# Kernel optimization log

Measured on AMD Instinct MI355X. Metric: run time of the kernel, lower is better.

Reference implementation:

```python
import jax, jax.numpy as jnp
import numpy as np

B, S, D, HW = 256, 32, 512, 196


def setup_inputs() -> dict:
    key = jax.random.key(0)
    ks = jax.random.split(key, 34)
    n = lambda k, sh, s=1.0: jax.random.normal(k, sh, dtype=jnp.float32) * s
    w = 0.03  # xavier-ish scale for D=512 layers
    return {
        "words": n(ks[0], (B, S, D)),
        "question": n(ks[1], (B, 2 * D)),
        "know": n(ks[2], (B, D, HW)),
        "control0": n(ks[3], (B, D)),
        "memory0": n(ks[4], (B, D)),
        # ControlUnit
        "Wsc": n(ks[5], (2 * D, D), w), "bsc": jnp.zeros((D,), jnp.float32),
        "Wp": n(ks[6], (D, D), w), "bp": jnp.zeros((D,), jnp.float32),
        "Wcq": n(ks[7], (2 * D, D), w), "bcq": jnp.zeros((D,), jnp.float32),
        "wac": n(ks[8], (D, 1), w), "bac": jnp.zeros((1,), jnp.float32),
        # ReadUnit
        "Wm": n(ks[9], (D, D), w), "bm": jnp.zeros((D,), jnp.float32),
        "Wk": n(ks[10], (D, D), w), "bk": jnp.zeros((D,), jnp.float32),
        "Wc1": n(ks[11], (3 * D, D), w), "bc1": jnp.zeros((D,), jnp.float32),
        "Wc2": n(ks[12], (D, D), w), "bc2": jnp.zeros((D,), jnp.float32),
        "war": n(ks[13], (D, 1), w), "bar": jnp.zeros((1,), jnp.float32),
        # WriteUnit (self-attention variant)
        "Wwc": n(ks[14], (D, D), w), "bwc": jnp.zeros((D,), jnp.float32),
        "waw": n(ks[15], (D, 1), w), "baw": jnp.zeros((1,), jnp.float32),
        "Wwcat": n(ks[16], (3 * D, D), w), "bwcat": jnp.zeros((D,), jnp.float32),
    }


def reference(words, question, know, control0, memory0,
              Wsc, bsc, Wp, bp, Wcq, bcq, wac, bac,
              Wm, bm, Wk, bk, Wc1, bc1, Wc2, bc2, war, bar,
              Wwc, bwc, waw, baw, Wwcat, bwcat):
    # ---- ControlUnit (step 0) ----
    q = jnp.tanh(question @ Wsc + bsc)                    # [B,D]
    pa = q @ Wp + bp                                      # position_aware[0]
    cq = jnp.concatenate([control0, pa], axis=1) @ Wcq + bcq  # [B,D]
    logit_c = (cq[:, None, :] * words) @ wac + bac        # [B,S,1]
    attn_c = jax.nn.softmax(logit_c, axis=1)
    control = jnp.sum(attn_c * words, axis=1)             # [B,D]

    # ---- ReadUnit ----
    pm = memory0 @ Wm + bm                                # [B,D]
    pk = jnp.einsum('bdn,de->ben', know, Wk) + bk[None, :, None]  # [B,D,HW]
    pm_b = jnp.broadcast_to(pm[:, :, None], pk.shape)
    feat = jnp.concatenate([pm_b * pk, pk, pm_b], axis=1)  # [B,3D,HW]
    h = jax.nn.relu(jnp.einsum('bfn,fd->bnd', feat, Wc1) + bc1)  # [B,HW,D]
    h = h @ Wc2 + bc2                                     # [B,HW,D]
    logit_r = (h * control[:, None, :]) @ war + bar       # [B,HW,1]
    a_r = jax.nn.softmax(logit_r[..., 0], axis=1)          # [B,HW]
    read = jnp.einsum('bdn,bn->bd', know, a_r)            # [B,D]

    # ---- WriteUnit (self-attention over previous controls; T=1 at step 0) ----
    sc = control @ Wwc + bwc                              # [B,D]
    ctrl_prev = control0[:, :, None]                      # [B,D,T]
    logit_w = jnp.einsum('bdt,d->bt', sc[:, :, None] * ctrl_prev, waw[:, 0]) + baw  # [B,T]
    a_w = jax.nn.softmax(logit_w, axis=1)
    attn_mem = jnp.einsum('bdt,bt->bd', memory0[:, :, None], a_w)  # [B,D]
    concat = jnp.concatenate([read, memory0, attn_mem], axis=1)    # [B,3D]
    next_mem = concat @ Wwcat + bwcat                     # [B,D]

    return control, next_mem
```

## Files before the change

### kernel.cpp

```cpp
#include <hip/hip_runtime.h>
#include <hip/hip_bf16.h>
#include <math.h>

typedef __hip_bfloat16 bf16;
typedef __attribute__((ext_vector_type(8))) short s8v;
typedef __attribute__((ext_vector_type(4))) short s4v;
typedef __attribute__((ext_vector_type(4))) float f4v;

#define BB 256
#define SS 32
#define DD 512
#define HWN 196
#define APW 72

__device__ __forceinline__ float b2f(bf16 x){ return __bfloat162float(x); }
__device__ __forceinline__ bf16 f2b(float x){ return __float2bfloat16(x); }
__device__ __forceinline__ float us2f(unsigned short u){
    union { unsigned int i; float f; } t; t.i = ((unsigned int)u) << 16; return t.f;
}
__device__ __forceinline__ float ldin(int dt, const void* p, size_t i){
    return dt ? b2f(((const bf16*)p)[i]) : ((const float*)p)[i];
}

__global__ void detect_k(const void* q, int* flag){
    __shared__ int cnt;
    if (threadIdx.x == 0) cnt = 0;
    __syncthreads();
    const unsigned short* u = (const unsigned short*)q;
    unsigned short v = u[threadIdx.x * 4];
    int e = (v >> 7) & 0xFF;
    atomicAdd(&cnt, (e >= 100 && e <= 140) ? 1 : 0);
    __syncthreads();
    if (threadIdx.x == 0) *flag = (cnt > 128) ? 1 : 0;
}

struct PJob { const void* s; const void* s_b; const void* s2; const void* s2_b;
              bf16* d; int R, C, ldd, kofs, mode, boff; };
struct PrepP { PJob j[11]; const void* war; const void* bk; float* warf; float* bkf; };

__global__ __launch_bounds__(256) void prep_k(PrepP P, const int* __restrict__ flag){
    const int dt = *flag;
    __shared__ float T[32][33];
    int bx = blockIdx.x;
    int ji = 0;
    #pragma unroll
    for (int i = 0; i < 11; ++i) if (bx >= P.j[i].boff) ji = i;
    PJob jb = P.j[ji];
    const void* src  = dt ? jb.s_b  : jb.s;
    const void* src2 = dt ? jb.s2_b : jb.s2;
    int t = bx - jb.boff;
    int tx = threadIdx.x & 31, ty = threadIdx.x >> 5;
    if (jb.mode == 3){
        for (int i = threadIdx.x; i < DD; i += 256){
            P.warf[i] = ldin(dt, P.war, i);
            P.bkf[i]  = ldin(dt, P.bk, i);
        }
        return;
    }
    int nrt = jb.R >> 5;
    int r0 = (t % nrt) << 5, c0 = (t / nrt) << 5;
    if (jb.mode == 2){
        for (int rr = ty; rr < 32; rr += 8)
            jb.d[(size_t)(r0 + rr) * jb.ldd + jb.kofs + c0 + tx] =
                f2b(ldin(dt, src, (size_t)(r0 + rr) * jb.C + c0 + tx));
        return;
    }
    for (int rr = ty; rr < 32; rr += 8){
        float v = ldin(dt, src, (size_t)(r0 + rr) * jb.C + c0 + tx);
        if (jb.mode == 1) v += ldin(dt, src2, (size_t)(r0 + rr) * jb.C + c0 + tx);
        T[rr][tx] = v;
    }
    __syncthreads();
    for (int rr = ty; rr < 32; rr += 8)
        jb.d[(size_t)(c0 + rr) * jb.ldd + jb.kofs + r0 + tx] = f2b(T[tx][rr]);
}

__global__ __launch_bounds__(256) void g1_mfma(const void* __restrict__ know,
                                               const bf16* __restrict__ BT,
                                               const float* __restrict__ bkf,
                                               bf16* __restrict__ C,
                                               int b0, int swz,
                                               const int* __restrict__ flag){
    const int dt = *flag;
    __shared__ __align__(16) bf16 As[128 * APW];
    __shared__ __align__(16) bf16 Bs[128 * APW];
    const int tid = threadIdx.x, lane = tid & 63, wave = tid >> 6;
    const int q = lane >> 4, mr = lane & 15;
    int idb = blockIdx.x, rt, ct;
    if (swz){ int g = idb >> 5, w = idb & 31; rt = g * 8 + (w & 7); ct = w >> 3; }
    else    { rt = idb >> 2; ct = idb & 3; }
    const int r0 = rt * 128, c0 = ct * 128;
    const int quad = tid >> 3;
    const int kg   = tid & 7;
    const int m    = r0 + quad * 4;
    const int bl   = m / HWN;
    const int n    = m - bl * HWN;
    const size_t abase = ((size_t)(b0 + bl) * DD) * HWN + n;
    f4v acc[2][8];
    #pragma unroll
    for (int t = 0; t < 2; ++t)
        #pragma unroll
        for (int j = 0; j < 8; ++j){ f4v z = {0.f,0.f,0.f,0.f}; acc[t][j] = z; }
    for (int k0 = 0; k0 < DD; k0 += 64){
        #pragma unroll
        for (int h = 0; h < 2; ++h){
            int kb = k0 + h * 32 + kg * 4;
            union { bf16 hh[4]; s4v v; } pk_[4];
            if (dt == 0){
                const float* kp = (const float*)know + abase + (size_t)kb * HWN;
                float4 ra  = *(const float4*)kp;
                float4 rb  = *(const float4*)(kp + HWN);
                float4 rc  = *(const float4*)(kp + 2 * HWN);
                float4 rd4 = *(const float4*)(kp + 3 * HWN);
                #pragma unroll
                for (int j = 0; j < 4; ++j){
                    pk_[j].hh[0] = f2b((&ra.x)[j]);
                    pk_[j].hh[1] = f2b((&rb.x)[j]);
                    pk_[j].hh[2] = f2b((&rc.x)[j]);
                    pk_[j].hh[3] = f2b((&rd4.x)[j]);
                }
            } else {
                const unsigned short* kp = (const unsigned short*)know + abase + (size_t)kb * HWN;
                ushort4 ua = *(const ushort4*)kp;
                ushort4 ub = *(const ushort4*)(kp + HWN);
                ushort4 uc = *(const ushort4*)(kp + 2 * HWN);
                ushort4 ud = *(const ushort4*)(kp + 3 * HWN);
                #pragma unroll
                for (int j = 0; j < 4; ++j){
                    ((unsigned short*)&pk_[j].v)[0] = (&ua.x)[j];
                    ((unsigned short*)&pk_[j].v)[1] = (&ub.x)[j];
                    ((unsigned short*)&pk_[j].v)[2] = (&uc.x)[j];
                    ((unsigned short*)&pk_[j].v)[3] = (&ud.x)[j];
                }
            }
            #pragma unroll
            for (int j = 0; j < 4; ++j)
                *(s4v*)&As[(quad * 4 + j) * APW + h * 32 + kg * 4] = pk_[j].v;
        }
        {
            int col = tid >> 1, kb = (tid & 1) * 32;
            const bf16* wp = BT + (size_t)(c0 + col) * DD + k0 + kb;
            bf16* dst = &Bs[col * APW + kb];
            #pragma unroll
            for (int t4 = 0; t4 < 32; t4 += 8)
                *(float4*)(dst + t4) = *(const float4*)(wp + t4);
        }
        __syncthreads();
        #pragma unroll
        for (int h = 0; h < 2; ++h){
            s8v a0 = *(const s8v*)&As[(wave * 32 + mr) * APW + h * 32 + q * 8];
            s8v a1 = *(const s8v*)&As[(wave * 32 + 16 + mr) * APW + h * 32 + q * 8];
            #pragma unroll
            for (int j = 0; j < 8; ++j){
                s8v b = *(const s8v*)&Bs[(j * 16 + mr) * APW + h * 32 + q * 8];
                acc[0][j] = __builtin_amdgcn_mfma_f32_16x16x32_bf16(a0, b, acc[0][j], 0, 0, 0);
                acc[1][j] = __builtin_amdgcn_mfma_f32_16x16x32_bf16(a1, b, acc[1][j], 0, 0, 0);
            }
        }
        __syncthreads();
    }
    #pragma unroll
    for (int t = 0; t < 2; ++t)
        #pragma unroll
        for (int j = 0; j < 8; ++j){
            float bb = bkf[c0 + j * 16 + mr];
            #pragma unroll
            for (int i = 0; i < 4; ++i){
                int row = r0 + wave * 32 + t * 16 + q * 4 + i;
                int col = c0 + j * 16 + mr;
                C[(size_t)row * DD + col] = f2b(acc[t][j][i] + bb);
            }
        }
}

__global__ __launch_bounds__(256) void g2_mfma(const bf16* __restrict__ Apk,
                                               const bf16* __restrict__ BT,
                                               const float* __restrict__ pmf,
                                               const float* __restrict__ t3b,
                                               const float* __restrict__ uf,
                                               float* __restrict__ lpart,
                                               int b0, int swz){
    __shared__ __align__(16) bf16 As[128 * APW];
    __shared__ __align__(16) bf16 Bs[128 * APW];
    const int tid = threadIdx.x, lane = tid & 63, wave = tid >> 6;
    const int q = lane >> 4, mr = lane & 15;
    int idb = blockIdx.x, u, ct;
    if (swz){ int g = idb >> 5, w = idb & 31; u = g * 8 + (w & 7); ct = w >> 3; }
    else    { u = idb >> 2; ct = idb & 3; }
    const int bl = u >> 1, rt = u & 1;
    const int b = b0 + bl;
    const int c0 = ct * 128, rbase = rt * 128;
    const float* pmb = pmf + (size_t)b * DD;
    f4v acc[2][8];
    #pragma unroll
    for (int t = 0; t < 2; ++t)
        #pragma unroll
        for (int j = 0; j < 8; ++j){ f4v z = {0.f,0.f,0.f,0.f}; acc[t][j] = z; }
    for (int k0 = 0; k0 < DD; k0 += 64){
        {
            int row = tid >> 1, kb = (tid & 1) * 32;
            int rl = rbase + row;
            bf16* dst = &As[row * APW + kb];
            if (rl < HWN){
                const bf16* ap = Apk + ((size_t)bl * HWN + rl) * DD + k0 + kb;
                #pragma unroll
                for (int t4 = 0; t4 < 32; t4 += 8)
                    *(float4*)(dst + t4) = *(const float4*)(ap + t4);
            } else {
                float4 z = {0.f,0.f,0.f,0.f};
                #pragma unroll
                for (int t4 = 0; t4 < 32; t4 += 8)
                    *(float4*)(dst + t4) = z;
            }
        }
        {
            int col = tid >> 1, kb = (tid & 1) * 32;
            const bf16* wrow = BT + (size_t)(c0 + col) * (2 * DD) + k0 + kb;
            bf16* dst = &Bs[col * APW + kb];
            #pragma unroll
            for (int t4 = 0; t4 < 32; t4 += 8){
                union { bf16 h[8]; float4 f; } w1, w2, be;
                w1.f = *(const float4*)(wrow + t4);
                w2.f = *(const float4*)(wrow + DD + t4);
                float4 pA = *(const float4*)(pmb + k0 + kb + t4);
                float4 pB = *(const float4*)(pmb + k0 + kb + t4 + 4);
                #pragma unroll
                for (int j = 0; j < 4; ++j){
                    be.h[j]     = f2b((&pA.x)[j] * b2f(w1.h[j])     + b2f(w2.h[j]));
                    be.h[4 + j] = f2b((&pB.x)[j] * b2f(w1.h[4 + j]) + b2f(w2.h[4 + j]));
                }
                *(float4*)(dst + t4) = be.f;
            }
        }
        __syncthreads();
        #pragma unroll
        for (int h = 0; h < 2; ++h){
            s8v a0 = *(const s8v*)&As[(wave * 32 + mr) * APW + h * 32 + q * 8];
            s8v a1 = *(const s8v*)&As[(wave * 32 + 16 + mr) * APW + h * 32 + q * 8];
            #pragma unroll
            for (int j = 0; j < 8; ++j){
                s8v b2 = *(const s8v*)&Bs[(j * 16 + mr) * APW + h * 32 + q * 8];
                acc[0][j] = __builtin_amdgcn_mfma_f32_16x16x32_bf16(a0, b2, acc[0][j], 0, 0, 0);
                acc[1][j] = __builtin_amdgcn_mfma_f32_16x16x32_bf16(a1, b2, acc[1][j], 0, 0, 0);
            }
        }
        __syncthreads();
    }
    float part[2][4] = {};
    #pragma unroll
    for (int t = 0; t < 2; ++t)
        #pragma unroll
        for (int j = 0; j < 8; ++j)
            #pragma unroll
            for (int i = 0; i < 4; ++i){
                int rl = rbase + wave * 32 + t * 16 + q * 4 + i;
                if (rl < HWN){
                    int col = c0 + j * 16 + mr;
                    float hv = acc[t][j][i] + t3b[(size_t)b * DD + col];
                    part[t][i] += fmaxf(hv, 0.f) * uf[(size_t)b * DD + col];
                }
            }
    #pragma unroll
    for (int t = 0; t < 2; ++t)
        #pragma unroll
        for (int i = 0; i < 4; ++i){
            float v = part[t][i];
            v += __shfl_xor(v, 1, 16);
            v += __shfl_xor(v, 2, 16);
            v += __shfl_xor(v, 4, 16);
            v += __shfl_xor(v, 8, 16);
            int rl = rbase + wave * 32 + t * 16 + q * 4 + i;
            if (mr == 0 && rl < HWN)
                lpart[(size_t)ct * (BB * HWN) + (size_t)b * HWN + rl] = v;
        }
}

struct SSeg { const void* A; int a_ws, lda, K, koff; };
struct SP {
    SSeg s[2]; int nseg;
    const bf16* BT; int ldb;
    const float* amul;
    const void* bias;
    float* C; int M, N, act;
    void* out2; int o2off;
};
struct SPP { SP j[2]; };

__global__ __launch_bounds__(256) void sgemm_k(SPP P, const int* __restrict__ flag){
    const int dt = *flag;
    const SP p = P.j[blockIdx.z];
    const int tid = threadIdx.x, lane = tid & 63, w = tid >> 6;
    const int q = lane >> 4, mr = lane & 15;
    const int n0 = blockIdx.x * 16, m0 = blockIdx.y * 64 + w * 16;
    f4v acc = {0.f,0.f,0.f,0.f};
    for (int sg = 0; sg < p.nseg; ++sg){
        const SSeg s = p.s[sg];
        const float* amul = (sg == 0) ? p.amul : nullptr;
        #pragma unroll 4
        for (int k0 = 0; k0 < s.K; k0 += 32){
            const int kk = k0 + q * 8;
            union { bf16 h[8]; s8v v; } a;
            if (s.a_ws || dt == 0){
                const float* Af = (const float*)s.A + (size_t)(m0 + mr) * s.lda + kk;
                float4 f0 = *(const float4*)Af;
                float4 f1 = *(const float4*)(Af + 4);
                float f[8] = {f0.x, f0.y, f0.z, f0.w, f1.x, f1.y, f1.z, f1.w};
                if (amul){
                    #pragma unroll
                    for (int j = 0; j < 8; ++j) f[j] *= amul[kk + j];
                }
                #pragma unroll
                for (int j = 0; j < 8; ++j) a.h[j] = f2b(f[j]);
            } else {
                a.v = *(const s8v*)((const bf16*)s.A + (size_t)(m0 + mr) * s.lda + kk);
                if (amul){
                    #pragma unroll
                    for (int j = 0; j < 8; ++j) a.h[j] = f2b(b2f(a.h[j]) * amul[kk + j]);
                }
            }
            s8v b = *(const s8v*)(p.BT + (size_t)(n0 + mr) * p.ldb + s.koff + kk);
            acc = __builtin_amdgcn_mfma_f32_16x16x32_bf16(a.v, b, acc, 0, 0, 0);
        }
    }
    #pragma unroll
    for (int i = 0; i < 4; ++i){
        int row = m0 + q * 4 + i, col = n0 + mr;
        float v = acc[i] + (p.bias ? ldin(dt, p.bias, col) : 0.f);
        if (p.act == 1) v = tanhf(v);
        p.C[(size_t)row * p.N + col] = v;
        if (p.out2){
            size_t oi = (size_t)p.o2off + (size_t)row * p.N + col;
            if (dt) ((bf16*)p.out2)[oi] = f2b(v);
            else    ((float*)p.out2)[oi] = v;
        }
    }
}

__global__ __launch_bounds__(256) void attn_control_k(const float* __restrict__ cq,
                                                      const void* __restrict__ wac,
                                                      const void* __restrict__ bac,
                                                      const void* __restrict__ words,
                                                      float* __restrict__ control,
                                                      const void* __restrict__ bc2,
                                                      const float* __restrict__ warf,
                                                      const void* __restrict__ bar,
                                                      float* __restrict__ bias_r,
                                                      void* __restrict__ out,
                                                      const int* __restrict__ flag){
    extern __shared__ float wl[];
    const int dt = *flag;
    const int b = blockIdx.x, tid = threadIdx.x;
    __shared__ float cw[DD];
    __shared__ float lg[SS];
    __shared__ float es[SS];
    __shared__ float red[256];
    for (int i = tid; i < SS * DD; i += 256)
        wl[i] = ldin(dt, words, (size_t)b * SS * DD + i);
    for (int d = tid; d < DD; d += 256) cw[d] = cq[(size_t)b*DD + d] * ldin(dt, wac, d);
    __syncthreads();
    int s = tid >> 3, l8 = tid & 7;
    float p = 0.f;
    for (int d = l8; d < DD; d += 8) p += cw[d] * wl[s * DD + d];
    for (int off = 4; off; off >>= 1) p += __shfl_down(p, off, 8);
    if (l8 == 0) lg[s] = p + ldin(dt, bac, 0);
    __syncthreads();
    if (tid < SS){
        float x = lg[tid];
        float mx = x;
        #pragma unroll
        for (int off = 16; off; off >>= 1) mx = fmaxf(mx, __shfl_xor(mx, off, 32));
        float e = expf(x - mx);
        float sm = e;
        #pragma unroll
        for (int off = 16; off; off >>= 1) sm += __shfl_xor(sm, off, 32);
        es[tid] = e / sm;
    }
    __syncthreads();
    float vb = 0.f;
    for (int d = tid; d < DD; d += 256){
        float c = 0.f;
        #pragma unroll 8
        for (int s2 = 0; s2 < SS; ++s2) c += es[s2] * wl[s2 * DD + d];
        control[(size_t)b*DD + d] = c;
        if (dt) ((bf16*)out)[(size_t)b*DD + d] = f2b(c);
        else    ((float*)out)[(size_t)b*DD + d] = c;
        vb += ldin(dt, bc2, d) * c * warf[d];
    }
    red[tid] = vb; __syncthreads();
    for (int off = 128; off; off >>= 1){ if (tid < off) red[tid] += red[tid + off]; __syncthreads(); }
    if (tid == 0) bias_r[b] = red[0] + ldin(dt, bar, 0);
}

__global__ __launch_bounds__(256) void softmax_read_k(const float* __restrict__ lpart,
                                                      const float* __restrict__ bias_r,
                                                      const void* __restrict__ know,
                                                      float* __restrict__ readout,
                                                      const int* __restrict__ flag){
    const int dt = *flag;
    const int b = blockIdx.x, tid = threadIdx.x;
    __shared__ float a[HWN];
    __shared__ float red[256];
    float x = -INFINITY;
    if (tid < HWN){
        float sacc = bias_r[b];
        #pragma unroll
        for (int c = 0; c < 4; ++c)
            sacc += lpart[(size_t)c * (BB * HWN) + (size_t)b * HWN + tid];
        x = sacc;
    }
    red[tid] = x; __syncthreads();
    for (int off = 128; off; off >>= 1){ if (tid < off) red[tid] = fmaxf(red[tid], red[tid + off]); __syncthreads(); }
    float mx = red[0]; __syncthreads();
    float e = (tid < HWN) ? expf(x - mx) : 0.f;
    red[tid] = e; __syncthreads();
    for (int off = 128; off; off >>= 1){ if (tid < off) red[tid] += red[tid + off]; __syncthreads(); }
    float inv = 1.f / red[0];
    if (tid < HWN) a[tid] = e * inv;
    __syncthreads();
    for (int d = tid; d < DD; d += 256){
        size_t base = ((size_t)b*DD + d) * HWN;
        float sum = 0.f;
        if (dt){
            const ushort4* k4 = (const ushort4*)((const unsigned short*)know + base);
            #pragma unroll 7
            for (int c = 0; c < HWN/4; ++c){
                ushort4 u4 = k4[c];
                sum += a[4*c+0]*us2f(u4.x) + a[4*c+1]*us2f(u4.y)
                     + a[4*c+2]*us2f(u4.z) + a[4*c+3]*us2f(u4.w);
            }
        } else {
            const float4* k4 = (const float4*)((const float*)know + base);
            #pragma unroll 7
            for (int c = 0; c < HWN/4; ++c){
                float4 f4 = k4[c];
                sum += a[4*c+0]*f4.x + a[4*c+1]*f4.y + a[4*c+2]*f4.z + a[4*c+3]*f4.w;
            }
        }
        readout[(size_t)b*DD + d] = sum;
    }
}

extern "C" void kernel_launch(void* const* d_in, const int* in_sizes, int n_in,
                              void* d_out, int out_size, void* d_ws, size_t ws_size,
                              hipStream_t stream){
    const void* words    = d_in[0];
    const void* question = d_in[1];
    const void* know     = d_in[2];
    const void* control0 = d_in[3];
    const void* memory0  = d_in[4];
    const void* Wsc = d_in[5];   const void* bsc = d_in[6];
    const void* Wp  = d_in[7];   const void* bp  = d_in[8];
    const void* Wcq = d_in[9];   const void* bcq = d_in[10];
    const void* wac = d_in[11];  const void* bac = d_in[12];
    const void* Wm  = d_in[13];  const void* bm  = d_in[14];
    const void* Wk  = d_in[15];  const void* bk  = d_in[16];
    const void* Wc1 = d_in[17];  const void* bc1 = d_in[18];
    const void* Wc2 = d_in[19];  const void* bc2 = d_in[20];
    const void* war = d_in[21];  const void* bar = d_in[22];
    const void* Wwcat = d_in[27]; const void* bwcat = d_in[28];

    int* flag = (int*)d_ws;
    float* F = ((float*)d_ws) + 16;
    const int NBD = BB * DD;
    float* q_   = F;
    float* pa   = F + 1*NBD;
    float* cq   = F + 2*NBD;
    float* ctrl = F + 3*NBD;
    float* pm   = F + 4*NBD;
    float* t3b  = F + 5*NBD;
    float* u_   = F + 6*NBD;
    float* rd   = F + 7*NBD;
    float* nm   = F + 8*NBD;
    float* bias_r = F + 9*NBD;
    float* warf   = bias_r + BB;
    float* bkf    = warf + DD;
    float* lpart  = bkf + DD;
    size_t off_f = 16 + 9*(size_t)NBD + BB + 2*DD + 8*(size_t)BB*HWN;
    size_t byte_off = (off_f * 4 + 255) & ~(size_t)255;
    bf16* WB = (bf16*)((char*)d_ws + byte_off);
    bf16* WscT   = WB;
    bf16* WcqT   = WscT  + (size_t)DD*2*DD;
    bf16* Wc1T2  = WcqT  + (size_t)DD*2*DD;
    bf16* WwcatF = Wc1T2 + (size_t)DD*2*DD;
    bf16* WpT    = WwcatF+ (size_t)DD*2*DD;
    bf16* WmT    = WpT   + (size_t)DD*DD;
    bf16* Wc1t3T = WmT   + (size_t)DD*DD;
    bf16* WkT    = Wc1t3T+ (size_t)DD*DD;
    bf16* Wc2cv  = WkT   + (size_t)DD*DD;
    size_t big_off = (byte_off + ((size_t)DD*2*DD*4 + (size_t)DD*DD*5) * sizeof(bf16) + 255) & ~(size_t)255;

    size_t per_batch = (size_t)HWN * DD * sizeof(bf16);
    size_t avail = (ws_size > big_off) ? (ws_size - big_off) : 0;
    int CB = (int)(avail / per_batch);
    CB &= ~31;
    if (CB > BB) CB = BB;
    if (CB < 32) CB = 32;
    bf16* pkT = (bf16*)((char*)d_ws + big_off);

    dim3 blk(256);

    {
        const int q_f32 = BB * 2 * DD * 4;
        const int q_b16 = BB * 2 * DD * 2;
        if (in_sizes[1] == q_f32)      (void)hipMemsetAsync(flag, 0, 4, stream);
        else if (in_sizes[1] == q_b16) (void)hipMemsetAsync(flag, 1, 4, stream);
        else detect_k<<<dim3(1), blk, 0, stream>>>(question, flag);
    }

    {
        PrepP P; int bo = 0;
        auto J = [&](const void* s, const void* sb, const void* s2, const void* s2b,
                     bf16* d, int R, int C, int ldd, int kofs, int mode, int idx){
            int nb = (mode == 3) ? 1 : ((R >> 5) * (C >> 5));
            P.j[idx] = PJob{ s, sb, s2, s2b, d, R, C, ldd, kofs, mode, bo };
            bo += nb;
        };
        const void* Wc1t3_f = (const void*)((const float*)Wc1 + (size_t)2*DD*DD);
        const void* Wc1t3_b = (const void*)((const bf16*) Wc1 + (size_t)2*DD*DD);
        const void* Ww1_f = (const void*)((const float*)Wwcat + (size_t)DD*DD);
        const void* Ww1_b = (const void*)((const bf16*) Wwcat + (size_t)DD*DD);
        const void* Ww2_f = (const void*)((const float*)Wwcat + (size_t)2*DD*DD);
        const void* Ww2_b = (const void*)((const bf16*) Wwcat + (size_t)2*DD*DD);
        J(Wsc,   Wsc,   nullptr, nullptr, WscT,   2*DD, DD, 2*DD, 0,   0, 0);
        J(Wp,    Wp,    nullptr, nullptr, WpT,    DD,   DD, DD,   0,   0, 1);
        J(Wcq,   Wcq,   nullptr, nullptr, WcqT,   2*DD, DD, 2*DD, 0,   0, 2);
        J(Wm,    Wm,    nullptr, nullptr, WmT,    DD,   DD, DD,   0,   0, 3);
        J(Wc1,   Wc1,   nullptr, nullptr, Wc1T2,  2*DD, DD, 2*DD, 0,   0, 4);
        J(Wc1t3_f, Wc1t3_b, nullptr, nullptr, Wc1t3T, DD, DD, DD, 0,   0, 5);
        J(Wk,    Wk,    nullptr, nullptr, WkT,    DD,   DD, DD,   0,   0, 6);
        J(Wwcat, Wwcat, nullptr, nullptr, WwcatF, DD,   DD, 2*DD, 0,   0, 7);
        J(Ww1_f, Ww1_b, Ww2_f,   Ww2_b,   WwcatF, DD,   DD, 2*DD, 512, 1, 8);
        J(Wc2,   Wc2,   nullptr, nullptr, Wc2cv,  DD,   DD, DD,   0,   2, 9);
        J(nullptr,nullptr,nullptr,nullptr,nullptr,0,    0,  0,    0,   3, 10);
        P.war = war; P.bk = bk; P.warf = warf; P.bkf = bkf;
        prep_k<<<dim3(bo), blk, 0, stream>>>(P, flag);
    }

    SPP P2;
    auto mkjob = [&](SP& p){ p = SP{}; };

    mkjob(P2.j[0]);
    P2.j[0].nseg = 1;
    P2.j[0].s[0] = SSeg{ question, 0, 2*DD, 2*DD, 0 };
    P2.j[0].BT = WscT; P2.j[0].ldb = 2*DD;
    P2.j[0].bias = bsc; P2.j[0].C = q_; P2.j[0].M = BB; P2.j[0].N = DD; P2.j[0].act = 1;
    mkjob(P2.j[1]);
    P2.j[1].nseg = 1;
    P2.j[1].s[0] = SSeg{ memory0, 0, DD, DD, 0 };
    P2.j[1].BT = WmT; P2.j[1].ldb = DD;
    P2.j[1].bias = bm; P2.j[1].C = pm; P2.j[1].M = BB; P2.j[1].N = DD; P2.j[1].act = 0;
    sgemm_k<<<dim3(DD/16, BB/64, 2), blk, 0, stream>>>(P2, flag);

    mkjob(P2.j[0]);
    P2.j[0].nseg = 1;
    P2.j[0].s[0] = SSeg{ q_, 1, DD, DD, 0 };
    P2.j[0].BT = WpT; P2.j[0].ldb = DD;
    P2.j[0].bias = bp; P2.j[0].C = pa; P2.j[0].M = BB; P2.j[0].N = DD; P2.j[0].act = 0;
    mkjob(P2.j[1]);
    P2.j[1].nseg = 1;
    P2.j[1].s[0] = SSeg{ pm, 1, DD, DD, 0 };
    P2.j[1].BT = Wc1t3T; P2.j[1].ldb = DD;
    P2.j[1].bias = bc1; P2.j[1].C = t3b; P2.j[1].M = BB; P2.j[1].N = DD; P2.j[1].act = 0;
    sgemm_k<<<dim3(DD/16, BB/64, 2), blk, 0, stream>>>(P2, flag);

    mkjob(P2.j[0]);
    P2.j[0].nseg = 2;
    P2.j[0].s[0] = SSeg{ control0, 0, DD, DD, 0 };
    P2.j[0].s[1] = SSeg{ pa,       1, DD, DD, 512 };
    P2.j[0].BT = WcqT; P2.j[0].ldb = 2*DD;
    P2.j[0].bias = bcq; P2.j[0].C = cq; P2.j[0].M = BB; P2.j[0].N = DD; P2.j[0].act = 0;
    sgemm_k<<<dim3(DD/16, BB/64, 1), blk, 0, stream>>>(P2, flag);

    {
        static bool attr_set = false;
        const int attn_lds = SS * DD * 4;
        if (!attr_set){
            (void)hipFuncSetAttribute(reinterpret_cast<const void*>(attn_control_k),
                                      hipFuncAttributeMaxDynamicSharedMemorySize, attn_lds);
            attr_set = true;
        }
        attn_control_k<<<dim3(BB), blk, attn_lds, stream>>>(cq, wac, bac, words, ctrl,
                                                            bc2, warf, bar, bias_r, d_out, flag);
    }

    mkjob(P2.j[0]);
    P2.j[0].nseg = 1;
    P2.j[0].s[0] = SSeg{ ctrl, 1, DD, DD, 0 };
    P2.j[0].BT = Wc2cv; P2.j[0].ldb = DD; P2.j[0].amul = warf;
    P2.j[0].C = u_; P2.j[0].M = BB; P2.j[0].N = DD; P2.j[0].act = 0;
    sgemm_k<<<dim3(DD/16, BB/64, 1), blk, 0, stream>>>(P2, flag);

    for (int b0 = 0; b0 < BB; b0 += CB){
        int cb = (b0 + CB <= BB) ? CB : (BB - b0);
        int M = cb * HWN;
        int nR = M / 128;
        int swz1 = (nR % 8 == 0) ? 1 : 0;
        g1_mfma<<<dim3(4 * nR), blk, 0, stream>>>(know, WkT, bkf, pkT, b0, swz1, flag);
        int nU = cb * 2;
        int swz2 = (nU % 8 == 0) ? 1 : 0;
        g2_mfma<<<dim3(4 * nU), blk, 0, stream>>>(pkT, Wc1T2, pm, t3b, u_, lpart, b0, swz2);
    }

    softmax_read_k<<<dim3(BB), blk, 0, stream>>>(lpart, bias_r, know, rd, flag);

    mkjob(P2.j[0]);
    P2.j[0].nseg = 2;
    P2.j[0].s[0] = SSeg{ rd,      1, DD, DD, 0 };
    P2.j[0].s[1] = SSeg{ memory0, 0, DD, DD, 512 };
    P2.j[0].BT = WwcatF; P2.j[0].ldb = 2*DD;
    P2.j[0].bias = bwcat; P2.j[0].C = nm; P2.j[0].M = BB; P2.j[0].N = DD; P2.j[0].act = 0;
    P2.j[0].out2 = d_out; P2.j[0].o2off = NBD;
    sgemm_k<<<dim3(DD/16, BB/64, 1), blk, 0, stream>>>(P2, flag);
}
```

Baseline: 559.1 us.

## XOR-swizzle MFMA LDS tiles and split softmax-read across channel blocks

Replaces the padded LDS layout (row stride 72) in both MFMA GEMM kernels with an unpadded 64-wide layout using an XOR swizzle on 16-byte slots, so tile reads and writes avoid bank conflicts while using less shared memory. Separately, softmax_read_k now launches 8 blocks per batch along y. Each block stages a 64-channel slice of know into LDS and reduces it with 4 threads per channel plus shuffles, instead of one thread streaming a whole 196-element row. The cost is that every y-block recomputes the softmax, and the 50KB LDS staging buffer limits occupancy.

```diff
diff --git a/kernel.cpp b/kernel.cpp
--- a/kernel.cpp
+++ b/kernel.cpp
@@ -11,7 +11,6 @@
 #define SS 32
 #define DD 512
 #define HWN 196
-#define APW 72
 
 __device__ __forceinline__ float b2f(bf16 x){ return __bfloat162float(x); }
 __device__ __forceinline__ bf16 f2b(float x){ return __float2bfloat16(x); }
@@ -20,6 +19,9 @@
 }
 __device__ __forceinline__ float ldin(int dt, const void* p, size_t i){
     return dt ? b2f(((const bf16*)p)[i]) : ((const float*)p)[i];
+}
+__device__ __forceinline__ int swz(int row, int slot){
+    return row * 64 + ((slot ^ (row & 7)) << 3);
 }
 
 __global__ void detect_k(const void* q, int* flag){
@@ -79,16 +81,16 @@
                                                const bf16* __restrict__ BT,
                                                const float* __restrict__ bkf,
                                                bf16* __restrict__ C,
-                                               int b0, int swz,
+                                               int b0, int swzb,
                                                const int* __restrict__ flag){
     const int dt = *flag;
-    __shared__ __align__(16) bf16 As[128 * APW];
-    __shared__ __align__(16) bf16 Bs[128 * APW];
+    __shared__ __align__(16) bf16 As[128 * 64];
+    __shared__ __align__(16) bf16 Bs[128 * 64];
     const int tid = threadIdx.x, lane = tid & 63, wave = tid >> 6;
     const int q = lane >> 4, mr = lane & 15;
     int idb = blockIdx.x, rt, ct;
-    if (swz){ int g = idb >> 5, w = idb & 31; rt = g * 8 + (w & 7); ct = w >> 3; }
-    else    { rt = idb >> 2; ct = idb & 3; }
+    if (swzb){ int g = idb >> 5, w = idb & 31; rt = g * 8 + (w & 7); ct = w >> 3; }
+    else     { rt = idb >> 2; ct = idb & 3; }
     const int r0 = rt * 128, c0 = ct * 128;
     const int quad = tid >> 3;
     const int kg   = tid & 7;
@@ -133,26 +135,28 @@
                     ((unsigned short*)&pk_[j].v)[3] = (&ud.x)[j];
                 }
             }
+            const int slot = h * 4 + (kg >> 1);
+            const int sub  = (kg & 1) * 4;
             #pragma unroll
             for (int j = 0; j < 4; ++j)
-                *(s4v*)&As[(quad * 4 + j) * APW + h * 32 + kg * 4] = pk_[j].v;
+                *(s4v*)&As[swz(quad * 4 + j, slot) + sub] = pk_[j].v;
         }
         {
-            int col = tid >> 1, kb = (tid & 1) * 32;
-            const bf16* wp = BT + (size_t)(c0 + col) * DD + k0 + kb;
-            bf16* dst = &Bs[col * APW + kb];
+            const int col = tid >> 1, sb = (tid & 1) * 4;
+            const bf16* wp = BT + (size_t)(c0 + col) * DD + k0 + (tid & 1) * 32;
             #pragma unroll
-            for (int t4 = 0; t4 < 32; t4 += 8)
-                *(float4*)(dst + t4) = *(const float4*)(wp + t4);
+            for (int t4 = 0; t4 < 4; ++t4)
+                *(float4*)&Bs[swz(col, sb + t4)] = *(const float4*)(wp + t4 * 8);
         }
         __syncthreads();
         #pragma unroll
         for (int h = 0; h < 2; ++h){
-            s8v a0 = *(const s8v*)&As[(wave * 32 + mr) * APW + h * 32 + q * 8];
-            s8v a1 = *(const s8v*)&As[(wave * 32 + 16 + mr) * APW + h * 32 + q * 8];
+            const int slot = h * 4 + q;
+            s8v a0 = *(const s8v*)&As[swz(wave * 32 + mr, slot)];
+            s8v a1 = *(const s8v*)&As[swz(wave * 32 + 16 + mr, slot)];
             #pragma unroll
             for (int j = 0; j < 8; ++j){
-                s8v b = *(const s8v*)&Bs[(j * 16 + mr) * APW + h * 32 + q * 8];
+                s8v b = *(const s8v*)&Bs[swz(j * 16 + mr, slot)];
                 acc[0][j] = __builtin_amdgcn_mfma_f32_16x16x32_bf16(a0, b, acc[0][j], 0, 0, 0);
                 acc[1][j] = __builtin_amdgcn_mfma_f32_16x16x32_bf16(a1, b, acc[1][j], 0, 0, 0);
             }
@@ -179,14 +183,14 @@
                                                const float* __restrict__ t3b,
                                                const float* __restrict__ uf,
                                                float* __restrict__ lpart,
-                                               int b0, int swz){
-    __shared__ __align__(16) bf16 As[128 * APW];
-    __shared__ __align__(16) bf16 Bs[128 * APW];
+                                               int b0, int swzb){
+    __shared__ __align__(16) bf16 As[128 * 64];
+    __shared__ __align__(16) bf16 Bs[128 * 64];
     const int tid = threadIdx.x, lane = tid & 63, wave = tid >> 6;
     const int q = lane >> 4, mr = lane & 15;
     int idb = blockIdx.x, u, ct;
-    if (swz){ int g = idb >> 5, w = idb & 31; u = g * 8 + (w & 7); ct = w >> 3; }
-    else    { u = idb >> 2; ct = idb & 3; }
+    if (swzb){ int g = idb >> 5, w = idb & 31; u = g * 8 + (w & 7); ct = w >> 3; }
+    else     { u = idb >> 2; ct = idb & 3; }
     const int bl = u >> 1, rt = u & 1;
     const int b = b0 + bl;
     const int c0 = ct * 128, rbase = rt * 128;
@@ -198,48 +202,48 @@
         for (int j = 0; j < 8; ++j){ f4v z = {0.f,0.f,0.f,0.f}; acc[t][j] = z; }
     for (int k0 = 0; k0 < DD; k0 += 64){
         {
-            int row = tid >> 1, kb = (tid & 1) * 32;
-            int rl = rbase + row;
-            bf16* dst = &As[row * APW + kb];
+            const int row = tid >> 1, sb = (tid & 1) * 4;
+            const int rl = rbase + row;
             if (rl < HWN){
-                const bf16* ap = Apk + ((size_t)bl * HWN + rl) * DD + k0 + kb;
+                const bf16* ap = Apk + ((size_t)bl * HWN + rl) * DD + k0 + (tid & 1) * 32;
                 #pragma unroll
-                for (int t4 = 0; t4 < 32; t4 += 8)
-                    *(float4*)(dst + t4) = *(const float4*)(ap + t4);
+                for (int t4 = 0; t4 < 4; ++t4)
+                    *(float4*)&As[swz(row, sb + t4)] = *(const float4*)(ap + t4 * 8);
             } else {
                 float4 z = {0.f,0.f,0.f,0.f};
                 #pragma unroll
-                for (int t4 = 0; t4 < 32; t4 += 8)
-                    *(float4*)(dst + t4) = z;
+                for (int t4 = 0; t4 < 4; ++t4)
+                    *(float4*)&As[swz(row, sb + t4)] = z;
             }
         }
         {
-            int col = tid >> 1, kb = (tid & 1) * 32;
-            const bf16* wrow = BT + (size_t)(c0 + col) * (2 * DD) + k0 + kb;
-            bf16* dst = &Bs[col * APW + kb];
+            const int col = tid >> 1, sb = (tid & 1) * 4;
+            const int kb = k0 + (tid & 1) * 32;
+            const bf16* wrow = BT + (size_t)(c0 + col) * (2 * DD) + kb;
             #pragma unroll
-            for (int t4 = 0; t4 < 32; t4 += 8){
+            for (int t4 = 0; t4 < 4; ++t4){
                 union { bf16 h[8]; float4 f; } w1, w2, be;
-                w1.f = *(const float4*)(wrow + t4);
-                w2.f = *(const float4*)(wrow + DD + t4);
-                float4 pA = *(const float4*)(pmb + k0 + kb + t4);
-                float4 pB = *(const float4*)(pmb + k0 + kb + t4 + 4);
+                w1.f = *(const float4*)(wrow + t4 * 8);
+                w2.f = *(const float4*)(wrow + DD + t4 * 8);
+                float4 pA = *(const float4*)(pmb + kb + t4 * 8);
+                float4 pB = *(const float4*)(pmb + kb + t4 * 8 + 4);
                 #pragma unroll
                 for (int j = 0; j < 4; ++j){
                     be.h[j]     = f2b((&pA.x)[j] * b2f(w1.h[j])     + b2f(w2.h[j]));
                     be.h[4 + j] = f2b((&pB.x)[j] * b2f(w1.h[4 + j]) + b2f(w2.h[4 + j]));
                 }
-                *(float4*)(dst + t4) = be.f;
+                *(float4*)&Bs[swz(col, sb + t4)] = be.f;
             }
         }
         __syncthreads();
         #pragma unroll
         for (int h = 0; h < 2; ++h){
-            s8v a0 = *(const s8v*)&As[(wave * 32 + mr) * APW + h * 32 + q * 8];
-            s8v a1 = *(const s8v*)&As[(wave * 32 + 16 + mr) * APW + h * 32 + q * 8];
+            const int slot = h * 4 + q;
+            s8v a0 = *(const s8v*)&As[swz(wave * 32 + mr, slot)];
+            s8v a1 = *(const s8v*)&As[swz(wave * 32 + 16 + mr, slot)];
             #pragma unroll
             for (int j = 0; j < 8; ++j){
-                s8v b2 = *(const s8v*)&Bs[(j * 16 + mr) * APW + h * 32 + q * 8];
+                s8v b2 = *(const s8v*)&Bs[swz(j * 16 + mr, slot)];
                 acc[0][j] = __builtin_amdgcn_mfma_f32_16x16x32_bf16(a0, b2, acc[0][j], 0, 0, 0);
                 acc[1][j] = __builtin_amdgcn_mfma_f32_16x16x32_bf16(a1, b2, acc[1][j], 0, 0, 0);
             }
@@ -397,9 +401,10 @@
                                                       float* __restrict__ readout,
                                                       const int* __restrict__ flag){
     const int dt = *flag;
-    const int b = blockIdx.x, tid = threadIdx.x;
+    const int b = blockIdx.x, ch = blockIdx.y, tid = threadIdx.x;
     __shared__ float a[HWN];
     __shared__ float red[256];
+    __shared__ float kl[64 * HWN];
     float x = -INFINITY;
     if (tid < HWN){
         float sacc = bias_r[b];
@@ -416,28 +421,31 @@
     for (int off = 128; off; off >>= 1){ if (tid < off) red[tid] += red[tid + off]; __syncthreads(); }
     float inv = 1.f / red[0];
     if (tid < HWN) a[tid] = e * inv;
+    const int d0 = ch * 64;
+    const size_t gbase = ((size_t)b * DD + d0) * HWN;
+    if (dt){
+        const ushort4* src = (const ushort4*)((const unsigned short*)know + gbase);
+        for (int i = tid; i < (64 * HWN) / 4; i += 256){
+            ushort4 u = src[i];
+            kl[4*i+0] = us2f(u.x); kl[4*i+1] = us2f(u.y);
+            kl[4*i+2] = us2f(u.z); kl[4*i+3] = us2f(u.w);
+        }
+    } else {
+        const float4* src = (const float4*)((const float*)know + gbase);
+        for (int i = tid; i < (64 * HWN) / 4; i += 256){
+            float4 f = src[i];
+            kl[4*i+0] = f.x; kl[4*i+1] = f.y; kl[4*i+2] = f.z; kl[4*i+3] = f.w;
+        }
+    }
     __syncthreads();
-    for (int d = tid; d < DD; d += 256){
-        size_t base = ((size_t)b*DD + d) * HWN;
-        float sum = 0.f;
-        if (dt){
-            const ushort4* k4 = (const ushort4*)((const unsigned short*)know + base);
-            #pragma unroll 7
-            for (int c = 0; c < HWN/4; ++c){
-                ushort4 u4 = k4[c];
-                sum += a[4*c+0]*us2f(u4.x) + a[4*c+1]*us2f(u4.y)
-                     + a[4*c+2]*us2f(u4.z) + a[4*c+3]*us2f(u4.w);
-            }
-        } else {
-            const float4* k4 = (const float4*)((const float*)know + base);
-            #pragma unroll 7
-            for (int c = 0; c < HWN/4; ++c){
-                float4 f4 = k4[c];
-                sum += a[4*c+0]*f4.x + a[4*c+1]*f4.y + a[4*c+2]*f4.z + a[4*c+3]*f4.w;
-            }
-        }
-        readout[(size_t)b*DD + d] = sum;
-    }
+    const int row = tid >> 2, part = tid & 3;
+    float p = 0.f;
+    const int nb = part * 49;
+    #pragma unroll 7
+    for (int n = 0; n < 49; ++n) p += a[nb + n] * kl[row * HWN + nb + n];
+    p += __shfl_xor(p, 1, 4);
+    p += __shfl_xor(p, 2, 4);
+    if (part == 0) readout[(size_t)b * DD + d0 + row] = p;
 }
 
 extern "C" void kernel_launch(void* const* d_in, const int* in_sizes, int n_in,
@@ -601,7 +609,7 @@
         g2_mfma<<<dim3(4 * nU), blk, 0, stream>>>(pkT, Wc1T2, pm, t3b, u_, lpart, b0, swz2);
     }
 
-    softmax_read_k<<<dim3(BB), blk, 0, stream>>>(lpart, bias_r, know, rd, flag);
+    softmax_read_k<<<dim3(BB, 8), blk, 0, stream>>>(lpart, bias_r, know, rd, flag);
 
     mkjob(P2.j[0]);
     P2.j[0].nseg = 2;
```

Measured after the change: 565.2 us. About the same (+1.1%).
